# Kernel optimization log

Hardware: AMD Instinct MI355X
Metric: run time of the kernel (lower is better)

Reference implementation:

```python
import jax, jax.numpy as jnp
import numpy as np

N_NODES = 100000
F_STATE = 64
HIDDEN = 256
N_EDGES = 1600000


def setup_inputs() -> dict:
    key = jax.random.key(0)
    ks = jax.random.split(key, 8)
    x = jax.random.normal(ks[0], (N_NODES, F_STATE), dtype=jnp.float32)
    edge_index = jax.random.randint(ks[1], (2, N_EDGES), 0, N_NODES, dtype=jnp.int32)
    # Pre-process MLP (1 layer): Dense(F_STATE -> HIDDEN), relu
    W_pre = jax.random.normal(ks[2], (F_STATE, HIDDEN), dtype=jnp.float32) / np.sqrt(F_STATE)
    b_pre = jnp.zeros((HIDDEN,), dtype=jnp.float32)
    # GeneralConv: Dense(HIDDEN -> HIDDEN), relu, then sum-aggregate message passing
    W_conv = jax.random.normal(ks[3], (HIDDEN, HIDDEN), dtype=jnp.float32) / np.sqrt(HIDDEN)
    b_conv = jnp.zeros((HIDDEN,), dtype=jnp.float32)
    # Post-process MLP (1 layer): Dense(2*HIDDEN -> F_STATE), activation=None
    W_post = jax.random.normal(ks[4], (2 * HIDDEN, F_STATE), dtype=jnp.float32) / np.sqrt(2 * HIDDEN)
    b_post = jnp.zeros((F_STATE,), dtype=jnp.float32)
    return {
        "x": x,
        "edge_index": edge_index,
        "W_pre": W_pre,
        "b_pre": b_pre,
        "W_conv": W_conv,
        "b_conv": b_conv,
        "W_post": W_post,
        "b_post": b_post,
        "steps": 4,
    }


def reference(x, edge_index, W_pre, b_pre, W_conv, b_conv, W_post, b_post, steps):
    n = x.shape[0]
    dst = edge_index[0]  # a.indices[:, 0] -> aggregation targets
    src = edge_index[1]  # a.indices[:, 1] -> message sources

    def step(h, _):
        p = jax.nn.relu(h @ W_pre + b_pre)                 # pre MLP     [N, H]
        m = jax.nn.relu(p @ W_conv + b_conv)               # conv dense  [N, H]
        z = jax.ops.segment_sum(m[src], dst, num_segments=n)  # sum agg  [N, H]
        out = jnp.concatenate([z, p], axis=-1) @ W_post + b_post  # cat-skip + post MLP (linear)
        return out, None

    out, _ = jax.lax.scan(step, x, None, length=steps)
    return out
```

## Files before the change

### kernel.cpp

```cpp
#include <hip/hip_runtime.h>


#define NN 100000
#define NPAD 100096
#define FS 64
#define HH 256
#define NE 1600000
#define NSTEPS 4
#define GA 128
#define EPB (NE / GA)
#define BK2SH 9
#define BS2 (1 << BK2SH)
#define NBK2 ((NN + BS2 - 1) / BS2)

typedef unsigned short u16;
typedef unsigned int u32;
typedef __attribute__((ext_vector_type(8))) short bfrag;
typedef __attribute__((ext_vector_type(4))) float ffrag;

static __device__ __forceinline__ u16 f2bf(float f) {
    union { float f; u32 u; } v; v.f = f;
    return (u16)((v.u + 0x7fffu + ((v.u >> 16) & 1u)) >> 16);
}
static __device__ __forceinline__ float bf2f(u16 h) {
    union { u32 u; float f; } v; v.u = (u32)h << 16; return v.f;
}
static __device__ __forceinline__ u32 pack2bf(float a, float b) {
    return (u32)f2bf(a) | ((u32)f2bf(b) << 16);
}

__global__ void cvt_x_k(const float4* __restrict__ x, uint2* __restrict__ hbf, int n4) {
    int i = blockIdx.x * 256 + threadIdx.x;
    if (i < n4) {
        float4 v = x[i];
        hbf[i] = make_uint2(pack2bf(v.x, v.y), pack2bf(v.z, v.w));
    }
}

__global__ void prep_w_k(const float* __restrict__ W_pre, const float* __restrict__ W_conv,
                         const float* __restrict__ W_post,
                         u16* __restrict__ Wpt, u16* __restrict__ Wct,
                         u16* __restrict__ Wzt, u16* __restrict__ Wp2t) {
    int i = blockIdx.x * 256 + threadIdx.x;
    if (i < 65536) {
        int c = i >> 8, k = i & 255;
        Wct[i] = f2bf(W_conv[k * HH + c]);
    } else if (i < 81920) {
        int j = i - 65536;
        int c = j >> 6, k = j & 63;
        Wpt[j] = f2bf(W_pre[k * HH + c]);
    } else if (i < 98304) {
        int j = i - 81920;
        int c = j >> 8, k = j & 255;
        Wzt[j] = f2bf(W_post[k * FS + c]);
    } else if (i < 114688) {
        int j = i - 98304;
        int c = j >> 8, k = j & 255;
        Wp2t[j] = f2bf(W_post[(HH + k) * FS + c]);
    }
}

__global__ __launch_bounds__(256) void fillA_k(const int* __restrict__ dst, const int* __restrict__ src,
                                               int* __restrict__ cntM, int* __restrict__ offM,
                                               u32* __restrict__ tmp) {
    __shared__ int cnt[256];
    __shared__ int sc[256];
    __shared__ int cur[256];
    const int t = threadIdx.x, b = blockIdx.x;
    const int e0 = b * EPB;
    cnt[t] = 0;
    __syncthreads();
    for (int i = t; i < EPB; i += 256) atomicAdd(&cnt[dst[e0 + i] >> BK2SH], 1);
    __syncthreads();
    int v = cnt[t];
    sc[t] = v;
    __syncthreads();
    for (int o = 1; o < 256; o <<= 1) {
        int y = (t >= o) ? sc[t - o] : 0;
        __syncthreads();
        sc[t] += y;
        __syncthreads();
    }
    int excl = sc[t] - v;
    cur[t] = excl;
    if (t < NBK2) {
        cntM[t * GA + b] = v;
        offM[t * GA + b] = excl;
    }
    __syncthreads();
    u32* seg = tmp + (size_t)b * EPB;
    for (int i = t; i < EPB; i += 256) {
        int d = dst[e0 + i], s = src[e0 + i];
        int pos = atomicAdd(&cur[d >> BK2SH], 1);
        seg[pos] = ((u32)(d & (BS2 - 1)) << 23) | (u32)s;
    }
}

__global__ void bscan_k(const int* __restrict__ cntM, int* __restrict__ bstart) {
    __shared__ int sh[256];
    const int t = threadIdx.x;
    int tot = 0;
    if (t < NBK2)
        for (int b = 0; b < GA; b++) tot += cntM[t * GA + b];
    sh[t] = tot;
    __syncthreads();
    for (int o = 1; o < 256; o <<= 1) {
        int y = (t >= o) ? sh[t - o] : 0;
        __syncthreads();
        sh[t] += y;
        __syncthreads();
    }
    if (t < NBK2) bstart[t] = sh[t] - tot;
    if (t == 255) bstart[NBK2] = sh[255];
}

__global__ __launch_bounds__(256) void fillB_k(const u32* __restrict__ tmp,
                                               const int* __restrict__ cntM, const int* __restrict__ offM,
                                               const int* __restrict__ bstart,
                                               int* __restrict__ offsets, int* __restrict__ srcs) {
    __shared__ int cnt[BS2];
    __shared__ int cur[BS2];
    __shared__ int runlen[GA];
    __shared__ int runoff[GA];
    const int t = threadIdx.x, k = blockIdx.x;
    const int nodeBase = k << BK2SH;
    cnt[t] = 0;
    cnt[t + 256] = 0;
    if (t < GA) {
        runlen[t] = cntM[k * GA + t];
        runoff[t] = offM[k * GA + t];
    }
    __syncthreads();
    const int rsub = t >> 6;
    const int elane = t & 63;
    for (int g = 0; g < GA / 4; g++) {
        int rb = g * 4 + rsub;
        int len = runlen[rb];
        const u32* run = tmp + (size_t)rb * EPB + runoff[rb];
        for (int e = elane; e < len; e += 64) atomicAdd(&cnt[run[e] >> 23], 1);
    }
    __syncthreads();
    int a = cnt[2 * t], b2 = cnt[2 * t + 1];
    int s = a + b2;
    cur[t] = s;
    __syncthreads();
    for (int o = 1; o < 256; o <<= 1) {
        int y = (t >= o) ? cur[t - o] : 0;
        __syncthreads();
        cur[t] += y;
        __syncthreads();
    }
    int exclPair = cur[t] - s;
    __syncthreads();
    const int base = bstart[k];
    int o0 = base + exclPair;
    int o1 = o0 + a;
    int n0 = nodeBase + 2 * t, n1 = n0 + 1;
    if (n0 < NN) offsets[n0] = o0;
    if (n1 < NN) offsets[n1] = o1;
    cur[2 * t] = o0;
    cur[2 * t + 1] = o1;
    __syncthreads();
    for (int g = 0; g < GA / 4; g++) {
        int rb = g * 4 + rsub;
        int len = runlen[rb];
        const u32* run = tmp + (size_t)rb * EPB + runoff[rb];
        for (int e = elane; e < len; e += 64) {
            u32 p = run[e];
            int pos = atomicAdd(&cur[p >> 23], 1);
            srcs[pos] = (int)(p & 0x7FFFFFu);
        }
    }
}

__global__ void final_off_k(int* __restrict__ offsets) {
    if (threadIdx.x == 0) offsets[NN] = NE;
}

__global__ __launch_bounds__(512, 4) void xform_k(const u16* __restrict__ hbf,
                                                  const u16* __restrict__ Wpt,
                                                  const float* __restrict__ b_pre,
                                                  const u16* __restrict__ Wct,
                                                  const float* __restrict__ b_conv,
                                                  const u16* __restrict__ Wzt,
                                                  const u16* __restrict__ Wp2t,
                                                  u16* __restrict__ qbf,
                                                  u16* __restrict__ pw2o) {
    __shared__ __align__(16) u16 ts[128 * 264];
    const int t = threadIdx.x;
    const int w = t >> 6, lane = t & 63;
    const int quad = lane >> 4, l16 = lane & 15;
    const int whi = w >> 2;
    const int cw = (w & 3) * 16;
    const int rh = whi * 64;
    const int nodeBase = blockIdx.x * 128;

    {
        ffrag acc[8][2];
#pragma unroll
        for (int mt = 0; mt < 8; mt++) { acc[mt][0] = (ffrag)0.f; acc[mt][1] = (ffrag)0.f; }
#pragma unroll
        for (int ch = 0; ch < 2; ch++) {
            const int kb = ch * 32 + quad * 8;
            bfrag b0 = *(const bfrag*)(Wpt + (size_t)(w * 32 + l16) * FS + kb);
            bfrag b1 = *(const bfrag*)(Wpt + (size_t)(w * 32 + 16 + l16) * FS + kb);
#pragma unroll
            for (int mt = 0; mt < 8; mt++) {
                bfrag a = *(const bfrag*)(hbf + (size_t)(nodeBase + mt * 16 + l16) * FS + kb);
                acc[mt][0] = __builtin_amdgcn_mfma_f32_16x16x32_bf16(a, b0, acc[mt][0], 0, 0, 0);
                acc[mt][1] = __builtin_amdgcn_mfma_f32_16x16x32_bf16(a, b1, acc[mt][1], 0, 0, 0);
            }
        }
#pragma unroll
        for (int nt = 0; nt < 2; nt++) {
            const int col = w * 32 + nt * 16 + l16;
            const float bv = b_pre[col];
#pragma unroll
            for (int mt = 0; mt < 8; mt++)
#pragma unroll
                for (int r = 0; r < 4; r++)
                    ts[(mt * 16 + quad * 4 + r) * 264 + col] = f2bf(fmaxf(acc[mt][nt][r] + bv, 0.f));
        }
    }
    __syncthreads();

    ffrag accm[8][2];
    ffrag accw[4];
    {
#pragma unroll
        for (int mt = 0; mt < 8; mt++) { accm[mt][0] = (ffrag)0.f; accm[mt][1] = (ffrag)0.f; }
#pragma unroll
        for (int mt = 0; mt < 4; mt++) accw[mt] = (ffrag)0.f;
#pragma unroll
        for (int ch = 0; ch < 8; ch++) {
            const int kb = ch * 32 + quad * 8;
            bfrag b0 = *(const bfrag*)(Wct + (size_t)(w * 32 + l16) * HH + kb);
            bfrag b1 = *(const bfrag*)(Wct + (size_t)(w * 32 + 16 + l16) * HH + kb);
            bfrag bw = *(const bfrag*)(Wp2t + (size_t)(cw + l16) * HH + kb);
            {
                bfrag a0 = *(const bfrag*)(ts + (0 * 16 + l16) * 264 + kb);
                bfrag a1 = *(const bfrag*)(ts + (1 * 16 + l16) * 264 + kb);
                bfrag a2 = *(const bfrag*)(ts + (2 * 16 + l16) * 264 + kb);
                bfrag a3 = *(const bfrag*)(ts + (3 * 16 + l16) * 264 + kb);
                if (whi == 0) {
                    accw[0] = __builtin_amdgcn_mfma_f32_16x16x32_bf16(a0, bw, accw[0], 0, 0, 0);
                    accw[1] = __builtin_amdgcn_mfma_f32_16x16x32_bf16(a1, bw, accw[1], 0, 0, 0);
                    accw[2] = __builtin_amdgcn_mfma_f32_16x16x32_bf16(a2, bw, accw[2], 0, 0, 0);
                    accw[3] = __builtin_amdgcn_mfma_f32_16x16x32_bf16(a3, bw, accw[3], 0, 0, 0);
                }
                accm[0][0] = __builtin_amdgcn_mfma_f32_16x16x32_bf16(a0, b0, accm[0][0], 0, 0, 0);
                accm[0][1] = __builtin_amdgcn_mfma_f32_16x16x32_bf16(a0, b1, accm[0][1], 0, 0, 0);
                accm[1][0] = __builtin_amdgcn_mfma_f32_16x16x32_bf16(a1, b0, accm[1][0], 0, 0, 0);
                accm[1][1] = __builtin_amdgcn_mfma_f32_16x16x32_bf16(a1, b1, accm[1][1], 0, 0, 0);
                accm[2][0] = __builtin_amdgcn_mfma_f32_16x16x32_bf16(a2, b0, accm[2][0], 0, 0, 0);
                accm[2][1] = __builtin_amdgcn_mfma_f32_16x16x32_bf16(a2, b1, accm[2][1], 0, 0, 0);
                accm[3][0] = __builtin_amdgcn_mfma_f32_16x16x32_bf16(a3, b0, accm[3][0], 0, 0, 0);
                accm[3][1] = __builtin_amdgcn_mfma_f32_16x16x32_bf16(a3, b1, accm[3][1], 0, 0, 0);
            }
            {
                bfrag a4 = *(const bfrag*)(ts + (4 * 16 + l16) * 264 + kb);
                bfrag a5 = *(const bfrag*)(ts + (5 * 16 + l16) * 264 + kb);
                bfrag a6 = *(const bfrag*)(ts + (6 * 16 + l16) * 264 + kb);
                bfrag a7 = *(const bfrag*)(ts + (7 * 16 + l16) * 264 + kb);
                if (whi == 1) {
                    accw[0] = __builtin_amdgcn_mfma_f32_16x16x32_bf16(a4, bw, accw[0], 0, 0, 0);
                    accw[1] = __builtin_amdgcn_mfma_f32_16x16x32_bf16(a5, bw, accw[1], 0, 0, 0);
                    accw[2] = __builtin_amdgcn_mfma_f32_16x16x32_bf16(a6, bw, accw[2], 0, 0, 0);
                    accw[3] = __builtin_amdgcn_mfma_f32_16x16x32_bf16(a7, bw, accw[3], 0, 0, 0);
                }
                accm[4][0] = __builtin_amdgcn_mfma_f32_16x16x32_bf16(a4, b0, accm[4][0], 0, 0, 0);
                accm[4][1] = __builtin_amdgcn_mfma_f32_16x16x32_bf16(a4, b1, accm[4][1], 0, 0, 0);
                accm[5][0] = __builtin_amdgcn_mfma_f32_16x16x32_bf16(a5, b0, accm[5][0], 0, 0, 0);
                accm[5][1] = __builtin_amdgcn_mfma_f32_16x16x32_bf16(a5, b1, accm[5][1], 0, 0, 0);
                accm[6][0] = __builtin_amdgcn_mfma_f32_16x16x32_bf16(a6, b0, accm[6][0], 0, 0, 0);
                accm[6][1] = __builtin_amdgcn_mfma_f32_16x16x32_bf16(a6, b1, accm[6][1], 0, 0, 0);
                accm[7][0] = __builtin_amdgcn_mfma_f32_16x16x32_bf16(a7, b0, accm[7][0], 0, 0, 0);
                accm[7][1] = __builtin_amdgcn_mfma_f32_16x16x32_bf16(a7, b1, accm[7][1], 0, 0, 0);
            }
        }
    }
    __syncthreads();

    {
#pragma unroll
        for (int nt = 0; nt < 2; nt++) {
            const int col = w * 32 + nt * 16 + l16;
            const float bv = b_conv[col];
#pragma unroll
            for (int mt = 0; mt < 8; mt++)
#pragma unroll
                for (int r = 0; r < 4; r++)
                    ts[(mt * 16 + quad * 4 + r) * 264 + col] = f2bf(fmaxf(accm[mt][nt][r] + bv, 0.f));
        }
    }
    __syncthreads();

    ffrag qa[4];
    {
#pragma unroll
        for (int mt = 0; mt < 4; mt++) qa[mt] = (ffrag)0.f;
#pragma unroll
        for (int ch = 0; ch < 8; ch++) {
            const int kb = ch * 32 + quad * 8;
            bfrag bz = *(const bfrag*)(Wzt + (size_t)(cw + l16) * HH + kb);
#pragma unroll
            for (int mt = 0; mt < 4; mt++) {
                bfrag am = *(const bfrag*)(ts + (rh + mt * 16 + l16) * 264 + kb);
                qa[mt] = __builtin_amdgcn_mfma_f32_16x16x32_bf16(am, bz, qa[mt], 0, 0, 0);
            }
        }
    }
    __syncthreads();

    {
        u16* stgP = ts;
        u16* stgQ = ts + 128 * 72;
#pragma unroll
        for (int mt = 0; mt < 4; mt++)
#pragma unroll
            for (int r = 0; r < 4; r++) {
                const int row = rh + mt * 16 + quad * 4 + r;
                stgP[row * 72 + cw + l16] = f2bf(accw[mt][r]);
                stgQ[row * 72 + cw + l16] = f2bf(qa[mt][r]);
            }
    }
    __syncthreads();

    {
        const u16* stgP = ts;
        const u16* stgQ = ts + 128 * 72;
#pragma unroll
        for (int s = 0; s < 2; s++) {
            const int j = t + s * 512;
            const int row = j >> 3, seg = j & 7;
            if (nodeBase + row < NN) {
                uint4 vp = *(const uint4*)(stgP + row * 72 + seg * 8);
                uint4 vq = *(const uint4*)(stgQ + row * 72 + seg * 8);
                *(uint4*)(pw2o + (size_t)(nodeBase + row) * FS + seg * 8) = vp;
                *(uint4*)(qbf + (size_t)(nodeBase + row) * FS + seg * 8) = vq;
            }
        }
    }
}

__global__ __launch_bounds__(256) void agg_k(const u32* __restrict__ q2,
                                             const int* __restrict__ offsets,
                                             const int* __restrict__ srcs,
                                             const u32* __restrict__ pw2,
                                             const float* __restrict__ b_post,
                                             u32* __restrict__ hbf_out,
                                             float* __restrict__ outf) {
    const int wave = threadIdx.x >> 6;
    const int lane = threadIdx.x & 63;
    const int node = blockIdx.x * 4 + wave;
    const int half = lane >> 5, c = lane & 31;
    const int beg = offsets[node], end = offsets[node + 1];
    float ax = 0.f, ay = 0.f, bx = 0.f, by = 0.f;
    int e = beg + half;
    for (; e + 6 < end; e += 8) {
        int s0 = srcs[e], s1 = srcs[e + 2], s2 = srcs[e + 4], s3 = srcs[e + 6];
        u32 g0 = q2[(size_t)s0 * 32 + c];
        u32 g1 = q2[(size_t)s1 * 32 + c];
        u32 g2 = q2[(size_t)s2 * 32 + c];
        u32 g3 = q2[(size_t)s3 * 32 + c];
        ax += bf2f((u16)g0) + bf2f((u16)g1);
        ay += bf2f((u16)(g0 >> 16)) + bf2f((u16)(g1 >> 16));
        bx += bf2f((u16)g2) + bf2f((u16)g3);
        by += bf2f((u16)(g2 >> 16)) + bf2f((u16)(g3 >> 16));
    }
    for (; e < end; e += 2) {
        u32 g = q2[(size_t)srcs[e] * 32 + c];
        ax += bf2f((u16)g);
        ay += bf2f((u16)(g >> 16));
    }
    ax += bx; ay += by;
    ax += __shfl_xor(ax, 32);
    ay += __shfl_xor(ay, 32);
    if (half == 0) {
        u32 wp = pw2[(size_t)node * 32 + c];
        float2 b = *(const float2*)&b_post[2 * c];
        float hx = ax + bf2f((u16)wp) + b.x;
        float hy = ay + bf2f((u16)(wp >> 16)) + b.y;
        if (outf) {
            *(float2*)&outf[(size_t)node * FS + 2 * c] = make_float2(hx, hy);
        } else {
            hbf_out[(size_t)node * 32 + c] = pack2bf(hx, hy);
        }
    }
}

extern "C" void kernel_launch(void* const* d_in, const int* in_sizes, int n_in,
                              void* d_out, int out_size, void* d_ws, size_t ws_size,
                              hipStream_t stream) {
    const float* x      = (const float*)d_in[0];
    const int*   ei     = (const int*)d_in[1];
    const float* W_pre  = (const float*)d_in[2];
    const float* b_pre  = (const float*)d_in[3];
    const float* W_conv = (const float*)d_in[4];
    const float* b_conv = (const float*)d_in[5];
    const float* W_post = (const float*)d_in[6];
    const float* b_post = (const float*)d_in[7];
    float* out = (float*)d_out;

    char* ws = (char*)d_ws;
    size_t off = 0;
    auto alloc = [&](size_t bytes) -> char* {
        char* r = ws + off;
        off += (bytes + 255) & ~(size_t)255;
        return r;
    };
    u16* hbf     = (u16*)alloc((size_t)NPAD * FS * 2);
    u16* qbf     = (u16*)alloc((size_t)NPAD * FS * 2);
    u16* pw2     = (u16*)alloc((size_t)NPAD * FS * 2);
    u32* tmp     = (u32*)alloc((size_t)NE * 4);
    int* offsets = (int*)alloc((size_t)(NN + 1) * 4);
    int* srcs    = (int*)alloc((size_t)NE * 4);
    int* cntM    = (int*)alloc((size_t)NBK2 * GA * 4);
    int* offM    = (int*)alloc((size_t)NBK2 * GA * 4);
    int* bstart  = (int*)alloc((size_t)(NBK2 + 1) * 4);
    u16* Wpt     = (u16*)alloc((size_t)HH * FS * 2);
    u16* Wct     = (u16*)alloc((size_t)HH * HH * 2);
    u16* Wzt     = (u16*)alloc((size_t)FS * HH * 2);
    u16* Wp2t    = (u16*)alloc((size_t)FS * HH * 2);
    (void)ws_size; (void)in_sizes; (void)n_in; (void)out_size;

    const int* dst = ei;
    const int* src = ei + NE;

    cvt_x_k<<<(NN * FS / 4 + 255) / 256, 256, 0, stream>>>((const float4*)x, (uint2*)hbf, NN * FS / 4);
    prep_w_k<<<448, 256, 0, stream>>>(W_pre, W_conv, W_post, Wpt, Wct, Wzt, Wp2t);

    fillA_k<<<GA, 256, 0, stream>>>(dst, src, cntM, offM, tmp);
    bscan_k<<<1, 256, 0, stream>>>(cntM, bstart);
    fillB_k<<<NBK2, 256, 0, stream>>>(tmp, cntM, offM, bstart, offsets, srcs);
    final_off_k<<<1, 64, 0, stream>>>(offsets);

    const int GB = (NN + 127) / 128;
    for (int s = 0; s < NSTEPS; s++) {
        xform_k<<<GB, 512, 0, stream>>>(hbf, Wpt, b_pre, Wct, b_conv, Wzt, Wp2t, qbf, pw2);
        if (s < NSTEPS - 1)
            agg_k<<<NN / 4, 256, 0, stream>>>((const u32*)qbf, offsets, srcs, (const u32*)pw2, b_post,
                                              (u32*)hbf, nullptr);
        else
            agg_k<<<NN / 4, 256, 0, stream>>>((const u32*)qbf, offsets, srcs, (const u32*)pw2, b_post,
                                              nullptr, out);
    }
}
```

Baseline: 605.3 us.

## Fuse neighbor aggregation into next step's dense transform kernel

Adds a fused kernel. Each block first gathers and sums neighbor messages for 64 nodes into shared memory, then runs the pre, conv and post matmuls on that tile with MFMA. This removes the bf16 hidden-state round trip through global memory and three kernel launches. Message buffers are double-buffered so the gather never reads rows being overwritten. The trade-off is that the gather now runs inside a heavy-shared-memory kernel with few blocks per CU and 16 serial nodes per wave, which can hurt latency hiding for the memory-bound gather.

```diff
diff --git a/kernel.cpp b/kernel.cpp
--- a/kernel.cpp
+++ b/kernel.cpp
@@ -343,12 +343,219 @@
     }
 }
 
+__global__ __launch_bounds__(256, 3) void fxform_k(const u32* __restrict__ qprev,
+                                                   const int* __restrict__ offsets,
+                                                   const int* __restrict__ srcs,
+                                                   const u32* __restrict__ pw2p,
+                                                   const float* __restrict__ b_post,
+                                                   const u16* __restrict__ Wpt,
+                                                   const float* __restrict__ b_pre,
+                                                   const u16* __restrict__ Wct,
+                                                   const float* __restrict__ b_conv,
+                                                   const u16* __restrict__ Wzt,
+                                                   const u16* __restrict__ Wp2t,
+                                                   u16* __restrict__ qbf,
+                                                   u16* __restrict__ pw2o) {
+    __shared__ __align__(16) char smem[52224];
+    u16* ts  = (u16*)smem;
+    u16* Hs  = (u16*)(smem + 33792);
+    u16* stB = (u16*)(smem + 43008);
+    const int t = threadIdx.x;
+    const int wave = t >> 6, lane = t & 63;
+    const int quad = lane >> 4, l16 = lane & 15;
+    const int half = lane >> 5, c = lane & 31;
+    const int nodeBase = blockIdx.x * 64;
+
+    {
+        u32* H32 = (u32*)Hs;
+        const float2 bp = *(const float2*)&b_post[2 * c];
+        for (int i = 0; i < 16; i++) {
+            const int node = nodeBase + wave * 16 + i;
+            float ax = 0.f, ay = 0.f, bx = 0.f, by = 0.f;
+            if (node < NN) {
+                const int beg = offsets[node], end = offsets[node + 1];
+                int e = beg + half;
+                for (; e + 6 < end; e += 8) {
+                    int s0 = srcs[e], s1 = srcs[e + 2], s2 = srcs[e + 4], s3 = srcs[e + 6];
+                    u32 g0 = qprev[(size_t)s0 * 32 + c];
+                    u32 g1 = qprev[(size_t)s1 * 32 + c];
+                    u32 g2 = qprev[(size_t)s2 * 32 + c];
+                    u32 g3 = qprev[(size_t)s3 * 32 + c];
+                    ax += bf2f((u16)g0) + bf2f((u16)g1);
+                    ay += bf2f((u16)(g0 >> 16)) + bf2f((u16)(g1 >> 16));
+                    bx += bf2f((u16)g2) + bf2f((u16)g3);
+                    by += bf2f((u16)(g2 >> 16)) + bf2f((u16)(g3 >> 16));
+                }
+                for (; e < end; e += 2) {
+                    u32 g = qprev[(size_t)srcs[e] * 32 + c];
+                    ax += bf2f((u16)g);
+                    ay += bf2f((u16)(g >> 16));
+                }
+            }
+            ax += bx; ay += by;
+            ax += __shfl_xor(ax, 32);
+            ay += __shfl_xor(ay, 32);
+            if (half == 0) {
+                float hx = 0.f, hy = 0.f;
+                if (node < NN) {
+                    u32 wp = pw2p[(size_t)node * 32 + c];
+                    hx = ax + bf2f((u16)wp) + bp.x;
+                    hy = ay + bf2f((u16)(wp >> 16)) + bp.y;
+                }
+                H32[(wave * 16 + i) * 36 + c] = pack2bf(hx, hy);
+            }
+        }
+    }
+    __syncthreads();
+
+    {
+        ffrag acc[4][4];
+#pragma unroll
+        for (int mt = 0; mt < 4; mt++)
+#pragma unroll
+            for (int nt = 0; nt < 4; nt++) acc[mt][nt] = (ffrag)0.f;
+#pragma unroll
+        for (int ch = 0; ch < 2; ch++) {
+            const int kb = ch * 32 + quad * 8;
+            bfrag a[4], b[4];
+#pragma unroll
+            for (int mt = 0; mt < 4; mt++)
+                a[mt] = *(const bfrag*)(Hs + (mt * 16 + l16) * 72 + kb);
+#pragma unroll
+            for (int nt = 0; nt < 4; nt++)
+                b[nt] = *(const bfrag*)(Wpt + (size_t)(wave * 64 + nt * 16 + l16) * FS + kb);
+#pragma unroll
+            for (int mt = 0; mt < 4; mt++)
+#pragma unroll
+                for (int nt = 0; nt < 4; nt++)
+                    acc[mt][nt] = __builtin_amdgcn_mfma_f32_16x16x32_bf16(a[mt], b[nt], acc[mt][nt], 0, 0, 0);
+        }
+#pragma unroll
+        for (int nt = 0; nt < 4; nt++) {
+            const int col = wave * 64 + nt * 16 + l16;
+            const float bv = b_pre[col];
+#pragma unroll
+            for (int mt = 0; mt < 4; mt++)
+#pragma unroll
+                for (int r = 0; r < 4; r++)
+                    ts[(mt * 16 + quad * 4 + r) * 264 + col] = f2bf(fmaxf(acc[mt][nt][r] + bv, 0.f));
+        }
+    }
+    __syncthreads();
+
+    ffrag accm[4][4];
+    ffrag accw[4];
+    {
+#pragma unroll
+        for (int mt = 0; mt < 4; mt++) {
+            accw[mt] = (ffrag)0.f;
+#pragma unroll
+            for (int nt = 0; nt < 4; nt++) accm[mt][nt] = (ffrag)0.f;
+        }
+        bfrag b[2][4], bw[2];
+        {
+            const int kb0 = quad * 8;
+#pragma unroll
+            for (int nt = 0; nt < 4; nt++)
+                b[0][nt] = *(const bfrag*)(Wct + (size_t)(wave * 64 + nt * 16 + l16) * HH + kb0);
+            bw[0] = *(const bfrag*)(Wp2t + (size_t)(wave * 16 + l16) * HH + kb0);
+        }
+#pragma unroll
+        for (int ch = 0; ch < 8; ch++) {
+            const int cur = ch & 1, nxt = cur ^ 1;
+            if (ch < 7) {
+                const int kb2 = (ch + 1) * 32 + quad * 8;
+#pragma unroll
+                for (int nt = 0; nt < 4; nt++)
+                    b[nxt][nt] = *(const bfrag*)(Wct + (size_t)(wave * 64 + nt * 16 + l16) * HH + kb2);
+                bw[nxt] = *(const bfrag*)(Wp2t + (size_t)(wave * 16 + l16) * HH + kb2);
+            }
+            const int kb = ch * 32 + quad * 8;
+            bfrag a[4];
+#pragma unroll
+            for (int mt = 0; mt < 4; mt++)
+                a[mt] = *(const bfrag*)(ts + (mt * 16 + l16) * 264 + kb);
+#pragma unroll
+            for (int mt = 0; mt < 4; mt++) {
+#pragma unroll
+                for (int nt = 0; nt < 4; nt++)
+                    accm[mt][nt] = __builtin_amdgcn_mfma_f32_16x16x32_bf16(a[mt], b[cur][nt], accm[mt][nt], 0, 0, 0);
+                accw[mt] = __builtin_amdgcn_mfma_f32_16x16x32_bf16(a[mt], bw[cur], accw[mt], 0, 0, 0);
+            }
+        }
+    }
+    __syncthreads();
+
+    {
+        u16* stA = Hs;
+#pragma unroll
+        for (int nt = 0; nt < 4; nt++) {
+            const int col = wave * 64 + nt * 16 + l16;
+            const float bv = b_conv[col];
+#pragma unroll
+            for (int mt = 0; mt < 4; mt++)
+#pragma unroll
+                for (int r = 0; r < 4; r++)
+                    ts[(mt * 16 + quad * 4 + r) * 264 + col] = f2bf(fmaxf(accm[mt][nt][r] + bv, 0.f));
+        }
+        const int colw = wave * 16 + l16;
+#pragma unroll
+        for (int mt = 0; mt < 4; mt++)
+#pragma unroll
+            for (int r = 0; r < 4; r++)
+                stA[(mt * 16 + quad * 4 + r) * 72 + colw] = f2bf(accw[mt][r]);
+    }
+    __syncthreads();
+
+#pragma unroll
+    for (int s = 0; s < 2; s++) {
+        const int j = t + s * 256;
+        const int row = j >> 3, seg = j & 7;
+        uint4 v = *(const uint4*)(Hs + row * 72 + seg * 8);
+        *(uint4*)(pw2o + (size_t)(nodeBase + row) * FS + seg * 8) = v;
+    }
+
+    {
+        ffrag qa[4];
+#pragma unroll
+        for (int mt = 0; mt < 4; mt++) qa[mt] = (ffrag)0.f;
+        bfrag bz[2];
+        bz[0] = *(const bfrag*)(Wzt + (size_t)(wave * 16 + l16) * HH + quad * 8);
+#pragma unroll
+        for (int ch = 0; ch < 8; ch++) {
+            const int cur = ch & 1;
+            if (ch < 7)
+                bz[cur ^ 1] = *(const bfrag*)(Wzt + (size_t)(wave * 16 + l16) * HH + (ch + 1) * 32 + quad * 8);
+            const int kb = ch * 32 + quad * 8;
+#pragma unroll
+            for (int mt = 0; mt < 4; mt++) {
+                bfrag am = *(const bfrag*)(ts + (mt * 16 + l16) * 264 + kb);
+                qa[mt] = __builtin_amdgcn_mfma_f32_16x16x32_bf16(am, bz[cur], qa[mt], 0, 0, 0);
+            }
+        }
+        const int col = wave * 16 + l16;
+#pragma unroll
+        for (int mt = 0; mt < 4; mt++)
+#pragma unroll
+            for (int r = 0; r < 4; r++)
+                stB[(mt * 16 + quad * 4 + r) * 72 + col] = f2bf(qa[mt][r]);
+    }
+    __syncthreads();
+
+#pragma unroll
+    for (int s = 0; s < 2; s++) {
+        const int j = t + s * 256;
+        const int row = j >> 3, seg = j & 7;
+        uint4 v = *(const uint4*)(stB + row * 72 + seg * 8);
+        *(uint4*)(qbf + (size_t)(nodeBase + row) * FS + seg * 8) = v;
+    }
+}
+
 __global__ __launch_bounds__(256) void agg_k(const u32* __restrict__ q2,
                                              const int* __restrict__ offsets,
                                              const int* __restrict__ srcs,
                                              const u32* __restrict__ pw2,
                                              const float* __restrict__ b_post,
-                                             u32* __restrict__ hbf_out,
                                              float* __restrict__ outf) {
     const int wave = threadIdx.x >> 6;
     const int lane = threadIdx.x & 63;
@@ -381,11 +588,7 @@
         float2 b = *(const float2*)&b_post[2 * c];
         float hx = ax + bf2f((u16)wp) + b.x;
         float hy = ay + bf2f((u16)(wp >> 16)) + b.y;
-        if (outf) {
-            *(float2*)&outf[(size_t)node * FS + 2 * c] = make_float2(hx, hy);
-        } else {
-            hbf_out[(size_t)node * 32 + c] = pack2bf(hx, hy);
-        }
+        *(float2*)&outf[(size_t)node * FS + 2 * c] = make_float2(hx, hy);
     }
 }
 
@@ -410,7 +613,8 @@
         return r;
     };
     u16* hbf     = (u16*)alloc((size_t)NPAD * FS * 2);
-    u16* qbf     = (u16*)alloc((size_t)NPAD * FS * 2);
+    u16* qA      = (u16*)alloc((size_t)NPAD * FS * 2);
+    u16* qB      = (u16*)alloc((size_t)NPAD * FS * 2);
     u16* pw2     = (u16*)alloc((size_t)NPAD * FS * 2);
     u32* tmp     = (u32*)alloc((size_t)NE * 4);
     int* offsets = (int*)alloc((size_t)(NN + 1) * 4);
@@ -435,14 +639,15 @@
     fillB_k<<<NBK2, 256, 0, stream>>>(tmp, cntM, offM, bstart, offsets, srcs);
     final_off_k<<<1, 64, 0, stream>>>(offsets);
 
-    const int GB = (NN + 127) / 128;
-    for (int s = 0; s < NSTEPS; s++) {
-        xform_k<<<GB, 512, 0, stream>>>(hbf, Wpt, b_pre, Wct, b_conv, Wzt, Wp2t, qbf, pw2);
-        if (s < NSTEPS - 1)
-            agg_k<<<NN / 4, 256, 0, stream>>>((const u32*)qbf, offsets, srcs, (const u32*)pw2, b_post,
-                                              (u32*)hbf, nullptr);
-        else
-            agg_k<<<NN / 4, 256, 0, stream>>>((const u32*)qbf, offsets, srcs, (const u32*)pw2, b_post,
-                                              nullptr, out);
-    }
-}
+    const int GB128 = (NN + 127) / 128;
+    const int GB64  = (NN + 63) / 64;
+
+    xform_k<<<GB128, 512, 0, stream>>>(hbf, Wpt, b_pre, Wct, b_conv, Wzt, Wp2t, qA, pw2);
+    fxform_k<<<GB64, 256, 0, stream>>>((const u32*)qA, offsets, srcs, (const u32*)pw2, b_post,
+                                       Wpt, b_pre, Wct, b_conv, Wzt, Wp2t, qB, pw2);
+    fxform_k<<<GB64, 256, 0, stream>>>((const u32*)qB, offsets, srcs, (const u32*)pw2, b_post,
+                                       Wpt, b_pre, Wct, b_conv, Wzt, Wp2t, qA, pw2);
+    fxform_k<<<GB64, 256, 0, stream>>>((const u32*)qA, offsets, srcs, (const u32*)pw2, b_post,
+                                       Wpt, b_pre, Wct, b_conv, Wzt, Wp2t, qB, pw2);
+    agg_k<<<NN / 4, 256, 0, stream>>>((const u32*)qB, offsets, srcs, (const u32*)pw2, b_post, out);
+}
```

Measured after the change: 836.8 us. 1.38x slower.
